# Kernel optimization log

Hardware: AMD Instinct MI355X
Metric: run time of the kernel (lower is better)

Reference implementation:

```python
import jax, jax.numpy as jnp
import numpy as np

E = 2048  # embed_size == seq_len (required: edge_weight_fc maps last dim E -> 1 on the NxN scores)
B = 4
N = 2048


def setup_inputs() -> dict:
    key = jax.random.key(0)
    ks = jax.random.split(key, 12)
    s = 0.02
    inp = {
        "query": jax.random.normal(ks[0], (B, N, E), jnp.float32),
        "key": jax.random.normal(ks[1], (B, N, E), jnp.float32),
        "value": jax.random.normal(ks[2], (B, N, E), jnp.float32),
        "mask": jax.random.randint(ks[3], (B, N, N), 0, 2, jnp.int32),
        # nn.Linear weights stored torch-style as [out, in]
        "Wq": jax.random.normal(ks[4], (E, E), jnp.float32) * s,
        "bq": jnp.zeros((E,), jnp.float32),
        "Wk": jax.random.normal(ks[5], (E, E), jnp.float32) * s,
        "bk": jnp.zeros((E,), jnp.float32),
        "Wv": jax.random.normal(ks[6], (E, E), jnp.float32) * s,
        "bv": jnp.zeros((E,), jnp.float32),
        "We": jax.random.normal(ks[7], (1, E), jnp.float32) * s,  # edge_weight_fc: Linear(E, 1)
        "be": jnp.zeros((1,), jnp.float32),
        "Wo": jax.random.normal(ks[8], (E, E), jnp.float32) * s,
        "bo": jnp.zeros((E,), jnp.float32),
    }
    return inp


def reference(query, key, value, mask, Wq, bq, Wk, bk, Wv, bv, We, be, Wo, bo):
    # QKV projections (torch Linear: x @ W.T + b)
    Q = query @ Wq.T + bq                       # [B, N, E]
    K = key @ Wk.T + bk                         # [B, N, E]
    V = value @ Wv.T + bv                       # [B, N, E]
    scale = 1.0 / jnp.sqrt(jnp.asarray(E, jnp.float32))
    scores = jnp.einsum("bqe,bke->bqk", Q, K) * scale   # [B, N, N]
    scores = scores + mask.astype(scores.dtype) * (-1e9)
    # graph_structure is non-None -> learned sigmoid edge gate over score rows
    edge_w = jax.nn.sigmoid(scores @ We.T + be)          # [B, N, 1]
    scores = scores * edge_w
    attn = jax.nn.softmax(scores, axis=-1)               # [B, N, N]
    # dropout is identity in eval mode
    out = jnp.einsum("bqk,bke->bqe", attn, V)            # [B, N, E]
    return out @ Wo.T + bo
```

## Files before the change

### kernel.cpp

```cpp
#include <hip/hip_runtime.h>
#include <math.h>

#define BB 4
#define NN 2048
#define EE 2048

typedef __attribute__((ext_vector_type(8))) unsigned short ushort8;
typedef __attribute__((ext_vector_type(8))) __bf16 bf16x8;
typedef __attribute__((ext_vector_type(4))) float f32x4;

__device__ __forceinline__ unsigned short f2bf(float f) {
  unsigned int u = __float_as_uint(f);
  u = u + 0x7fffu + ((u >> 16) & 1u);
  return (unsigned short)(u >> 16);
}
__device__ __forceinline__ float bf2f(unsigned short h) {
  return __uint_as_float((unsigned)h << 16);
}

__device__ __forceinline__ void gload16(const void* g, void* l) {
  __builtin_amdgcn_global_load_lds(
      (__attribute__((address_space(1))) void*)g,
      (__attribute__((address_space(3))) void*)l, 16, 0, 0);
}

#define BARRIER() __builtin_amdgcn_s_barrier()
#define WAIT_VM(N) asm volatile("s_waitcnt vmcnt(" #N ")")

__global__ __launch_bounds__(256) void k_f32_to_bf16(const float* __restrict__ in,
                                                     unsigned short* __restrict__ out) {
  size_t i = (size_t)blockIdx.x * 256 + threadIdx.x;
  const float4* ip = (const float4*)in;
  float4 a = ip[i * 2];
  float4 b = ip[i * 2 + 1];
  ushort8 o;
  o[0] = f2bf(a.x); o[1] = f2bf(a.y); o[2] = f2bf(a.z); o[3] = f2bf(a.w);
  o[4] = f2bf(b.x); o[5] = f2bf(b.y); o[6] = f2bf(b.z); o[7] = f2bf(b.w);
  *((ushort8*)out + i) = o;
}

__global__ __launch_bounds__(256) void k_conv3(const float* __restrict__ s0,
                                               const float* __restrict__ s1,
                                               const float* __restrict__ s2,
                                               unsigned short* __restrict__ d0,
                                               unsigned short* __restrict__ d1,
                                               unsigned short* __restrict__ d2) {
  const float* in; unsigned short* out;
  if (blockIdx.z == 0) { in = s0; out = d0; }
  else if (blockIdx.z == 1) { in = s1; out = d1; }
  else { in = s2; out = d2; }
  size_t i = (size_t)blockIdx.x * 256 + threadIdx.x;
  const float4* ip = (const float4*)in;
  float4 a = ip[i * 2];
  float4 b = ip[i * 2 + 1];
  ushort8 o;
  o[0] = f2bf(a.x); o[1] = f2bf(a.y); o[2] = f2bf(a.z); o[3] = f2bf(a.w);
  o[4] = f2bf(b.x); o[5] = f2bf(b.y); o[6] = f2bf(b.z); o[7] = f2bf(b.w);
  *((ushort8*)out + i) = o;
}

__global__ __launch_bounds__(256) void k_trf2b3(const float* __restrict__ s0,
                                                const float* __restrict__ s1,
                                                const float* __restrict__ s2,
                                                unsigned short* __restrict__ d0,
                                                unsigned short* __restrict__ d1,
                                                unsigned short* __restrict__ d2) {
  __shared__ __attribute__((aligned(16))) unsigned short tile[64][72];
  const float* in; unsigned short* out;
  if (blockIdx.z == 0) { in = s0; out = d0; }
  else if (blockIdx.z == 1) { in = s1; out = d1; }
  else { in = s2; out = d2; }
  const long eb = (long)blockIdx.x * 64;
  const long nb = (long)blockIdx.y * 64;
  const int t = threadIdx.x;
  const int r = t >> 3;
  const int c = (t & 7) * 8;

  const float* p0 = in + (nb + r) * (long)EE + eb + c;
  const float* p1 = in + (nb + 32 + r) * (long)EE + eb + c;
  float4 a0 = *(const float4*)p0, a1 = *(const float4*)(p0 + 4);
  float4 b0 = *(const float4*)p1, b1 = *(const float4*)(p1 + 4);
  unsigned short* t0 = &tile[r][c];
  unsigned short* t1 = &tile[r + 32][c];
  t0[0] = f2bf(a0.x); t0[1] = f2bf(a0.y); t0[2] = f2bf(a0.z); t0[3] = f2bf(a0.w);
  t0[4] = f2bf(a1.x); t0[5] = f2bf(a1.y); t0[6] = f2bf(a1.z); t0[7] = f2bf(a1.w);
  t1[0] = f2bf(b0.x); t1[1] = f2bf(b0.y); t1[2] = f2bf(b0.z); t1[3] = f2bf(b0.w);
  t1[4] = f2bf(b1.x); t1[5] = f2bf(b1.y); t1[6] = f2bf(b1.z); t1[7] = f2bf(b1.w);
  __syncthreads();
  ushort8 o0, o1;
#pragma unroll
  for (int j = 0; j < 8; j++) { o0[j] = tile[c + j][r]; o1[j] = tile[c + j][r + 32]; }
  *(ushort8*)(out + (eb + r) * (long)NN + nb + c) = o0;
  *(ushort8*)(out + (eb + r + 32) * (long)NN + nb + c) = o1;
}

__global__ __launch_bounds__(256) void k_transpose(const unsigned short* __restrict__ in,
                                                   unsigned short* __restrict__ out) {
  __shared__ __attribute__((aligned(16))) unsigned short tile[64][72];
  const long z = blockIdx.z;
  const long eb = (long)blockIdx.x * 64;
  const long nb = (long)blockIdx.y * 64;
  const unsigned short* ip = in + z * (long)NN * EE;
  unsigned short* op = out + z * (long)NN * EE;
  const int t = threadIdx.x;
  const int r = t >> 3;
  const int c = (t & 7) * 8;

  ushort8 u0 = *(const ushort8*)(ip + (nb + r) * EE + eb + c);
  ushort8 u1 = *(const ushort8*)(ip + (nb + 32 + r) * EE + eb + c);
  *(ushort8*)&tile[r][c] = u0;
  *(ushort8*)&tile[r + 32][c] = u1;
  __syncthreads();
  ushort8 o0, o1;
#pragma unroll
  for (int j = 0; j < 8; j++) { o0[j] = tile[c + j][r]; o1[j] = tile[c + j][r + 32]; }
  *(ushort8*)(op + (eb + r) * NN + nb + c) = o0;
  *(ushort8*)(op + (eb + r + 32) * NN + nb + c) = o1;
}

__global__ __launch_bounds__(256) void k_vecw(const float* __restrict__ Wq,
                                              const float* __restrict__ Wk,
                                              const float* __restrict__ bq,
                                              const float* __restrict__ bk,
                                              float* __restrict__ u,
                                              float* __restrict__ w2b,
                                              float* __restrict__ t4) {
  const int e = blockIdx.x * 256 + threadIdx.x;
  const int tt0 = blockIdx.y * 64;
  float su = 0.f, sw = 0.f;
#pragma unroll 4
  for (int i = 0; i < 64; i++) {
    int tt = tt0 + i;
    su += Wq[(long)tt * EE + e] * bk[tt];
    sw += Wk[(long)tt * EE + e] * bq[tt];
  }
  atomicAdd(&u[e], su);
  atomicAdd(&w2b[e], sw);
  if (blockIdx.x == 0 && threadIdx.x < 64) {
    int lane = threadIdx.x;
    float p = bq[tt0 + lane] * bk[tt0 + lane];
    for (int off = 32; off >= 1; off >>= 1) p += __shfl_down(p, off);
    if (lane == 0) atomicAdd(t4, p);
  }
}

__global__ __launch_bounds__(256) void k_cvec(const float* __restrict__ Wo,
                                              const float* __restrict__ bv,
                                              const float* __restrict__ bo,
                                              float* __restrict__ cv) {
  int row = blockIdx.x * 4 + (threadIdx.x >> 6);
  int lane = threadIdx.x & 63;
  float s = 0.f;
  for (int j = lane; j < EE; j += 64) s += Wo[(long)row * EE + j] * bv[j];
  for (int off = 32; off >= 1; off >>= 1) s += __shfl_down(s, off);
  if (lane == 0) cv[row] = s + bo[row];
}

__global__ __launch_bounds__(256) void k_rowterm(const unsigned short* __restrict__ qb,
                                                 const float* __restrict__ u,
                                                 const float* __restrict__ t4,
                                                 float* __restrict__ rt) {
  long row = (long)blockIdx.x * 4 + (threadIdx.x >> 6);
  int lane = threadIdx.x & 63;
  const unsigned short* qr = qb + row * EE;
  float s = 0.f;
#pragma unroll
  for (int it = 0; it < 4; ++it) {
    int e0 = it * 512 + lane * 8;
    ushort8 qv = *(const ushort8*)(qr + e0);
#pragma unroll
    for (int j = 0; j < 8; j++) s += bf2f(qv[j]) * u[e0 + j];
  }
  for (int off = 32; off >= 1; off >>= 1) s += __shfl_down(s, off);
  if (lane == 0) rt[row] = s + *t4;
}

__global__ __launch_bounds__(512, 4) void k_gemm128(
    const unsigned short* __restrict__ A, long lda, long sA,
    const unsigned short* __restrict__ Bm, long ldb, long sB,
    unsigned short* __restrict__ Co, long ldc, long sC, int K) {
  __shared__ __attribute__((aligned(16))) unsigned short As[2 * 8192];
  __shared__ __attribute__((aligned(16))) unsigned short Bs[2 * 8192];
  const int gx = gridDim.x, gy = gridDim.y;
  int lin = (int)blockIdx.x + gx * ((int)blockIdx.y + gy * (int)blockIdx.z);
  int nwg = gx * gy * (int)gridDim.z;
  int chunk = nwg >> 3;
  int sw = (lin & 7) * chunk + (lin >> 3);
  int bz = sw / (gx * gy); int rem = sw - bz * (gx * gy);
  int by = rem / gx; int bx = rem - by * gx;

  const long m0 = (long)by * 128;
  const long n0 = (long)bx * 128;
  const unsigned short* Ab = A + (long)bz * sA;
  const unsigned short* Bb = Bm + (long)bz * sB;
  const int t = threadIdx.x;
  const int lane = t & 63;
  const int w = t >> 6;
  const int wm = w >> 2, wn = w & 3;

  const int srow = t >> 3;
  const int scol = (((t & 7) * 16) ^ (((t >> 5) & 1) << 5)) >> 1;
  const unsigned short* Ga = Ab + (m0 + srow) * lda + scol;
  const unsigned short* Gb = Bb + (n0 + srow) * ldb + scol;
  const int ldst = t * 8;

#define STAGE(buf, tile) do { \
    const unsigned short* ga_ = Ga + (long)(tile) * 64; \
    const unsigned short* gb_ = Gb + (long)(tile) * 64; \
    unsigned short* la_ = As + (buf) * 8192 + ldst; \
    unsigned short* lb_ = Bs + (buf) * 8192 + ldst; \
    gload16(ga_, la_); gload16(ga_ + 64 * lda, la_ + 4096); \
    gload16(gb_, lb_); gload16(gb_ + 64 * ldb, lb_ + 4096); \
  } while (0)

  const int r = lane & 15;
  const int q = lane >> 4;
  const int rb2 = ((r * 128 + q * 16) ^ ((r & 4) << 3)) >> 1;
  const int aBase = wm * 4096 + rb2;
  const int bBase = wn * 2048 + rb2;

  f32x4 acc[4][2] = {};
  bf16x8 a[4][2], b[2][2];
  const int J = K >> 6;
  STAGE(0, 0);
  WAIT_VM(0);
  BARRIER();
  for (int j = 0; j < J; ++j) {
    const int c = j & 1;
    const unsigned short* Ac = As + c * 8192;
    const unsigned short* Bc = Bs + c * 8192;
#pragma unroll
    for (int mi = 0; mi < 4; mi++)
#pragma unroll
      for (int kk = 0; kk < 2; kk++)
        a[mi][kk] = *(const bf16x8*)(Ac + aBase + mi * 1024 + kk * 32);
#pragma unroll
    for (int ni = 0; ni < 2; ni++)
#pragma unroll
      for (int kk = 0; kk < 2; kk++)
        b[ni][kk] = *(const bf16x8*)(Bc + bBase + ni * 1024 + kk * 32);
    if (j + 1 < J) STAGE(c ^ 1, j + 1);
    __builtin_amdgcn_s_setprio(1);
#pragma unroll
    for (int mi = 0; mi < 4; mi++)
#pragma unroll
      for (int ni = 0; ni < 2; ni++)
#pragma unroll
        for (int kk = 0; kk < 2; kk++)
          acc[mi][ni] = __builtin_amdgcn_mfma_f32_16x16x32_bf16(
              a[mi][kk], b[ni][kk], acc[mi][ni], 0, 0, 0);
    __builtin_amdgcn_s_setprio(0);
    WAIT_VM(0);
    BARRIER();
  }
#undef STAGE
  const int cr0 = wm * 64 + (q << 2);
  const int cc0 = wn * 32 + r;
#pragma unroll
  for (int mi = 0; mi < 4; mi++)
#pragma unroll
    for (int rr = 0; rr < 4; rr++) {
      long row = m0 + cr0 + mi * 16 + rr;
#pragma unroll
      for (int ni = 0; ni < 2; ni++)
        Co[(long)bz * sC + row * ldc + n0 + cc0 + ni * 16] = f2bf(acc[mi][ni][rr]);
    }
}

template <int EPI>
__global__ __launch_bounds__(512, 2) void k_gemm256(
    const unsigned short* __restrict__ A, long lda, long sA,
    const unsigned short* __restrict__ Bm, long ldb, long sB,
    void* __restrict__ Cv, long ldc, long sC, int K,
    const float* __restrict__ bias,
    const int* __restrict__ mask, long sMask,
    const float* __restrict__ rt, float scale,
    const float* __restrict__ We, float* __restrict__ edot) {
  __shared__ __attribute__((aligned(16))) unsigned short As[2 * 16384];
  __shared__ __attribute__((aligned(16))) unsigned short Bs[2 * 16384];

  const int gx = gridDim.x, gy = gridDim.y;
  int lin = (int)blockIdx.x + gx * ((int)blockIdx.y + gy * (int)blockIdx.z);
  int nwg = gx * gy * (int)gridDim.z;
  int chunk = nwg >> 3;
  int sw = (lin & 7) * chunk + (lin >> 3);
  int bz = sw / (gx * gy); int rem = sw - bz * (gx * gy);
  int by = rem / gx; int bx = rem - by * gx;

  const long m0 = (long)by * 256;
  const long n0 = (long)bx * 256;
  const unsigned short* Ab = A + (long)bz * sA;
  const unsigned short* Bb = Bm + (long)bz * sB;

  const int t = threadIdx.x;
  const int lane = t & 63;
  const int w = t >> 6;
  const int wm = w >> 2;
  const int wn = w & 3;

  const int p0 = t * 16;
  const int q0 = p0 ^ (((p0 >> 9) & 1) << 5);
  const int srow = ((q0 >> 10) >> 1) * 16 + ((q0 >> 6) & 15);
  const int scol = ((q0 >> 10) & 1) * 32 + ((q0 & 63) >> 1);
  const unsigned short* Ga = Ab + (m0 + srow) * lda + scol;
  const unsigned short* Gb = Bb + (n0 + srow) * ldb + scol;
  const int ldst = t * 8;

#define STAGE_A(buf, h, tile) do { \
    const unsigned short* g_ = Ga + (long)(tile) * 64 + (long)(h) * 128 * lda; \
    unsigned short* l_ = As + (buf) * 16384 + (h) * 8192 + ldst; \
    gload16(g_, l_); gload16(g_ + 64 * lda, l_ + 4096); \
  } while (0)
#define STAGE_B(buf, h, tile) do { \
    const unsigned short* g_ = Gb + (long)(tile) * 64 + (long)(h) * 128 * ldb; \
    unsigned short* l_ = Bs + (buf) * 16384 + (h) * 8192 + ldst; \
    gload16(g_, l_); gload16(g_ + 64 * ldb, l_ + 4096); \
  } while (0)

  const int r = lane & 15;
  const int q = lane >> 4;
  const int c2h = ((q * 16) ^ (((lane >> 3) & 1) << 5)) >> 1;
  const int aBase = wm * 8192 + r * 32 + c2h;
  const int bBase = (wn >> 1) * 8192 + (wn & 1) * 4096 + r * 32 + c2h;

#define RD_A(bp, mbase) do { \
    _Pragma("unroll") for (int mi = 0; mi < 4; mi++) \
    _Pragma("unroll") for (int kk = 0; kk < 2; kk++) \
      a[mi][kk] = *(const bf16x8*)((bp) + aBase + ((mbase) + mi) * 1024 + kk * 512); \
  } while (0)
#define RD_B(bp, nbase) do { \
    _Pragma("unroll") for (int ni = 0; ni < 2; ni++) \
    _Pragma("unroll") for (int kk = 0; kk < 2; kk++) \
      b[(nbase) + ni][kk] = *(const bf16x8*)((bp) + bBase + ((nbase) + ni) * 1024 + kk * 512); \
  } while (0)
#define MFMA_Q(mbase, nbase) do { \
    BARRIER(); \
    __builtin_amdgcn_s_setprio(1); \
    _Pragma("unroll") for (int mi = 0; mi < 4; mi++) \
    _Pragma("unroll") for (int ni = 0; ni < 2; ni++) \
    _Pragma("unroll") for (int kk = 0; kk < 2; kk++) \
      acc[(mbase) + mi][(nbase) + ni] = __builtin_amdgcn_mfma_f32_16x16x32_bf16( \
          a[mi][kk], b[(nbase) + ni][kk], acc[(mbase) + mi][(nbase) + ni], 0, 0, 0); \
    __builtin_amdgcn_s_setprio(0); \
    BARRIER(); \
  } while (0)

  f32x4 acc[8][4] = {};
  bf16x8 a[4][2], b[4][2];
  const unsigned short* A0 = As;
  const unsigned short* B0 = Bs;
  const unsigned short* A1 = As + 16384;
  const unsigned short* B1 = Bs + 16384;
  const int J = K >> 7;

  STAGE_B(0, 0, 0); STAGE_B(0, 1, 0);
  STAGE_A(0, 0, 0); STAGE_A(0, 1, 0);
  STAGE_B(1, 0, 1); STAGE_B(1, 1, 1);
  WAIT_VM(4);
  BARRIER();

  for (int j = 0; j < J; ++j) {
    const int t0 = 2 * j, t1 = 2 * j + 1;
    const bool pf = (j + 1 < J);

    RD_A(A0, 0); RD_B(B0, 0);
    STAGE_A(1, 0, t1);
    MFMA_Q(0, 0);

    RD_B(B0, 2);
    STAGE_A(1, 1, t1);
    MFMA_Q(0, 2);

    RD_A(A0, 4);
    if (pf) STAGE_B(0, 0, t0 + 2);
    MFMA_Q(4, 0);

    if (pf) { STAGE_B(0, 1, t0 + 2); WAIT_VM(4); } else { WAIT_VM(0); }
    MFMA_Q(4, 2);

    RD_A(A1, 0); RD_B(B1, 0);
    if (pf) STAGE_A(0, 0, t0 + 2);
    MFMA_Q(0, 0);

    RD_B(B1, 2);
    if (pf) STAGE_A(0, 1, t0 + 2);
    MFMA_Q(0, 2);

    RD_A(A1, 4);
    if (pf) STAGE_B(1, 0, t1 + 2);
    MFMA_Q(4, 0);

    if (pf) { STAGE_B(1, 1, t1 + 2); WAIT_VM(4); }
    MFMA_Q(4, 2);
  }
#undef STAGE_A
#undef STAGE_B
#undef RD_A
#undef RD_B
#undef MFMA_Q

  const int cr0 = wm * 128 + (q << 2);
  const int cc0 = wn * 64 + r;
  if (EPI == 0) {
    unsigned short* Co = (unsigned short*)Cv + (long)bz * sC;
#pragma unroll
    for (int mi = 0; mi < 8; mi++)
#pragma unroll
      for (int rr = 0; rr < 4; rr++) {
        long row = m0 + cr0 + mi * 16 + rr;
#pragma unroll
        for (int ni = 0; ni < 4; ni++) {
          long col = n0 + cc0 + ni * 16;
          float v = acc[mi][ni][rr];
          if (bias) v += bias[col];
          Co[row * ldc + col] = f2bf(v);
        }
      }
  } else if (EPI == 1) {
    unsigned short* Co = (unsigned short*)Cv + (long)bz * sC;
    const int* Mp = mask + (long)bz * sMask;
    const float* rtb = rt + (long)bz * NN;
    float* edpart = (float*)As;
    if (t < 256) edpart[t] = 0.f;
    __syncthreads();
    float wec[4];
#pragma unroll
    for (int ni = 0; ni < 4; ni++) wec[ni] = We[n0 + cc0 + ni * 16];
#pragma unroll
    for (int mi = 0; mi < 8; mi++) {
      float pr[4];
#pragma unroll
      for (int rr = 0; rr < 4; rr++) {
        long row = m0 + cr0 + mi * 16 + rr;
        float rv = rtb[row];
        float pv = 0.f;
#pragma unroll
        for (int ni = 0; ni < 4; ni++) {
          long col = n0 + cc0 + ni * 16;
          float sm = (acc[mi][ni][rr] + rv) * scale + (float)Mp[row * ldc + col] * -1e9f;
          Co[row * ldc + col] = f2bf(sm);
          pv += sm * wec[ni];
        }
        pr[rr] = pv;
      }
#pragma unroll
      for (int mask_ = 1; mask_ < 16; mask_ <<= 1)
#pragma unroll
        for (int rr = 0; rr < 4; rr++) pr[rr] += __shfl_xor(pr[rr], mask_);
      if (r == 0) {
#pragma unroll
        for (int rr = 0; rr < 4; rr++)
          atomicAdd(&edpart[cr0 + mi * 16 + rr], pr[rr]);
      }
    }
    __syncthreads();
    if (t < 256) atomicAdd(&edot[(long)bz * NN + m0 + t], edpart[t]);
  } else {
    float* Co = (float*)Cv + (long)bz * sC;
#pragma unroll
    for (int mi = 0; mi < 8; mi++)
#pragma unroll
      for (int rr = 0; rr < 4; rr++) {
        long row = m0 + cr0 + mi * 16 + rr;
#pragma unroll
        for (int ni = 0; ni < 4; ni++) {
          long col = n0 + cc0 + ni * 16;
          Co[row * ldc + col] = acc[mi][ni][rr] + bias[col];
        }
      }
  }
}

__global__ __launch_bounds__(256) void k_edge_softmax(unsigned short* __restrict__ attn,
                                                      const float* __restrict__ edot,
                                                      const float* __restrict__ be) {
  __shared__ float r2[4], r3[4];
  const long row = blockIdx.x;
  unsigned short* srow = attn + row * (long)NN;
  const int t = threadIdx.x;
  const int lane = t & 63;
  const int w = t >> 6;

  float edge = 1.0f / (1.0f + expf(-(edot[row] + be[0])));
  ushort8 v = *(const ushort8*)(srow + t * 8);
  float s[8];
  float mx = -3.4e38f;
#pragma unroll
  for (int j = 0; j < 8; j++) { s[j] = bf2f(v[j]) * edge; mx = fmaxf(mx, s[j]); }
#pragma unroll
  for (int off = 32; off >= 1; off >>= 1) mx = fmaxf(mx, __shfl_down(mx, off));
  if (lane == 0) r2[w] = mx;
  __syncthreads();
  mx = fmaxf(fmaxf(r2[0], r2[1]), fmaxf(r2[2], r2[3]));

  float sum = 0.f;
  float p[8];
#pragma unroll
  for (int j = 0; j < 8; j++) { p[j] = expf(s[j] - mx); sum += p[j]; }
#pragma unroll
  for (int off = 32; off >= 1; off >>= 1) sum += __shfl_down(sum, off);
  if (lane == 0) r3[w] = sum;
  __syncthreads();
  sum = r3[0] + r3[1] + r3[2] + r3[3];
  float inv = 1.0f / sum;

  ushort8 o;
#pragma unroll
  for (int j = 0; j < 8; j++) o[j] = f2bf(p[j] * inv);
  *(ushort8*)(srow + t * 8) = o;
}

extern "C" void kernel_launch(void* const* d_in, const int* in_sizes, int n_in,
                              void* d_out, int out_size, void* d_ws, size_t ws_size,
                              hipStream_t stream) {
  (void)in_sizes; (void)n_in; (void)out_size; (void)ws_size;
  const float* query = (const float*)d_in[0];
  const float* key_  = (const float*)d_in[1];
  const float* value = (const float*)d_in[2];
  const int*   mask  = (const int*)d_in[3];
  const float* Wq = (const float*)d_in[4];
  const float* bq = (const float*)d_in[5];
  const float* Wk = (const float*)d_in[6];
  const float* bk = (const float*)d_in[7];
  const float* Wv = (const float*)d_in[8];
  const float* bv = (const float*)d_in[9];
  const float* We = (const float*)d_in[10];
  const float* be = (const float*)d_in[11];
  const float* Wo = (const float*)d_in[12];
  const float* bo = (const float*)d_in[13];
  float* out = (float*)d_out;

  const long WSZ = (long)EE * EE;
  char* ws = (char*)d_ws;
  unsigned short* WkT = (unsigned short*)(ws);
  unsigned short* Wob = WkT + WSZ;
  unsigned short* WqT = WkT + 2 * WSZ;
  unsigned short* WvT = WkT + 3 * WSZ;
  unsigned short* W2T = (unsigned short*)(ws + 33554432L);
  unsigned short* W3T = W2T + WSZ;
  unsigned short* attn = (unsigned short*)(ws);
  unsigned short* qb  = (unsigned short*)(ws + 79691776L);
  unsigned short* kb  = (unsigned short*)(ws + 114294784L);
  unsigned short* vb  = (unsigned short*)(ws + 148897792L);
  unsigned short* Tb  = vb;
  unsigned short* Vt2 = (unsigned short*)(ws + 183500800L);
  unsigned short* Vt2T = qb;
  float* cvec = (float*)(ws + 219938816L);
  float* uvec = cvec + EE;
  float* w2b  = cvec + 2 * EE;
  float* t4   = cvec + 3 * EE;
  float* rt   = cvec + 3 * EE + 64;
  float* edot = rt + (long)BB * NN;

  const float scale = 1.0f / sqrtf((float)EE);
  dim3 blk(256), blk5(512);

  k_trf2b3<<<dim3(32, 32, 3), blk, 0, stream>>>(Wk, Wq, Wv, WkT, WqT, WvT);
  k_f32_to_bf16<<<2048, blk, 0, stream>>>(Wo, Wob);
  hipMemsetAsync(uvec, 0, (2 * EE + 64) * sizeof(float), stream);
  hipMemsetAsync(edot, 0, (long)BB * NN * sizeof(float), stream);
  k_vecw<<<dim3(8, 32), blk, 0, stream>>>(Wq, Wk, bq, bk, uvec, w2b, t4);
  k_cvec<<<512, blk, 0, stream>>>(Wo, bv, bo, cvec);
  k_gemm128<<<dim3(16, 16, 2), blk5, 0, stream>>>(WkT, EE, WSZ, WqT, EE, WSZ,
      W2T, EE, WSZ, EE);
  k_conv3<<<dim3(8192, 1, 3), blk, 0, stream>>>(query, key_, value, qb, kb, vb);
  k_gemm256<0><<<dim3(8, 32, 1), blk5, 0, stream>>>(vb, EE, 0, W3T, EE, 0,
      Vt2, EE, 0, EE, nullptr, nullptr, 0, nullptr, 0.f, nullptr, nullptr);
  k_gemm256<0><<<dim3(8, 32, 1), blk5, 0, stream>>>(qb, EE, 0, W2T, EE, 0,
      Tb, EE, 0, EE, w2b, nullptr, 0, nullptr, 0.f, nullptr, nullptr);
  k_rowterm<<<2048, blk, 0, stream>>>(qb, uvec, t4, rt);
  k_transpose<<<dim3(32, 32, BB), blk, 0, stream>>>(Vt2, Vt2T);
  k_gemm256<1><<<dim3(8, 8, BB), blk5, 0, stream>>>(Tb, EE, (long)NN * EE, kb, EE, (long)NN * EE,
      attn, NN, (long)NN * NN, EE, nullptr, mask, (long)NN * NN, rt, scale, We, edot);
  k_edge_softmax<<<BB * NN, blk, 0, stream>>>(attn, edot, be);
  k_gemm256<2><<<dim3(8, 8, BB), blk5, 0, stream>>>(attn, NN, (long)NN * NN,
      Vt2T, NN, (long)EE * NN, out, EE, (long)NN * EE, NN,
      cvec, nullptr, 0, nullptr, 0.f, nullptr, nullptr);
}
```

Measured before the change: 471.0 us.

## Replace pipelined 256x256 GEMM with simple single-buffered 128x128 tile kernel

Replaces the heavily pipelined, double-buffered 256x256 GEMM kernel (512 threads, swizzled LDS, interleaved prefetch and MFMA phases) with a plain 128x128 tile kernel. The new kernel uses 256 threads, a single 32-wide K step, and two syncthreads per iteration. Launch grids are rescaled to match. This gives up load/compute overlap and data reuse, and the unswizzled LDS reads may bank-conflict, which likely makes all four big GEMMs slower. It reads like a simpler baseline or experiment.

```diff
diff --git a/kernel.cpp b/kernel.cpp
--- a/kernel.cpp
+++ b/kernel.cpp
@@ -268,7 +268,7 @@
 }
 
 template <int EPI>
-__global__ __launch_bounds__(512, 2) void k_gemm256(
+__global__ __launch_bounds__(256) void k_gemm97(
     const unsigned short* __restrict__ A, long lda, long sA,
     const unsigned short* __restrict__ Bm, long ldb, long sB,
     void* __restrict__ Cv, long ldc, long sC, int K,
@@ -276,8 +276,8 @@
     const int* __restrict__ mask, long sMask,
     const float* __restrict__ rt, float scale,
     const float* __restrict__ We, float* __restrict__ edot) {
-  __shared__ __attribute__((aligned(16))) unsigned short As[2 * 16384];
-  __shared__ __attribute__((aligned(16))) unsigned short Bs[2 * 16384];
+  __shared__ __attribute__((aligned(16))) unsigned short As[128 * 32];
+  __shared__ __attribute__((aligned(16))) unsigned short Bs[128 * 32];
 
   const int gx = gridDim.x, gy = gridDim.y;
   int lin = (int)blockIdx.x + gx * ((int)blockIdx.y + gy * (int)blockIdx.z);
@@ -287,130 +287,65 @@
   int bz = sw / (gx * gy); int rem = sw - bz * (gx * gy);
   int by = rem / gx; int bx = rem - by * gx;
 
-  const long m0 = (long)by * 256;
-  const long n0 = (long)bx * 256;
+  const long m0 = (long)by * 128;
+  const long n0 = (long)bx * 128;
   const unsigned short* Ab = A + (long)bz * sA;
   const unsigned short* Bb = Bm + (long)bz * sB;
 
   const int t = threadIdx.x;
   const int lane = t & 63;
   const int w = t >> 6;
-  const int wm = w >> 2;
-  const int wn = w & 3;
-
-  const int p0 = t * 16;
-  const int q0 = p0 ^ (((p0 >> 9) & 1) << 5);
-  const int srow = ((q0 >> 10) >> 1) * 16 + ((q0 >> 6) & 15);
-  const int scol = ((q0 >> 10) & 1) * 32 + ((q0 & 63) >> 1);
-  const unsigned short* Ga = Ab + (m0 + srow) * lda + scol;
-  const unsigned short* Gb = Bb + (n0 + srow) * ldb + scol;
-  const int ldst = t * 8;
-
-#define STAGE_A(buf, h, tile) do { \
-    const unsigned short* g_ = Ga + (long)(tile) * 64 + (long)(h) * 128 * lda; \
-    unsigned short* l_ = As + (buf) * 16384 + (h) * 8192 + ldst; \
-    gload16(g_, l_); gload16(g_ + 64 * lda, l_ + 4096); \
-  } while (0)
-#define STAGE_B(buf, h, tile) do { \
-    const unsigned short* g_ = Gb + (long)(tile) * 64 + (long)(h) * 128 * ldb; \
-    unsigned short* l_ = Bs + (buf) * 16384 + (h) * 8192 + ldst; \
-    gload16(g_, l_); gload16(g_ + 64 * ldb, l_ + 4096); \
-  } while (0)
-
-  const int r = lane & 15;
-  const int q = lane >> 4;
-  const int c2h = ((q * 16) ^ (((lane >> 3) & 1) << 5)) >> 1;
-  const int aBase = wm * 8192 + r * 32 + c2h;
-  const int bBase = (wn >> 1) * 8192 + (wn & 1) * 4096 + r * 32 + c2h;
-
-#define RD_A(bp, mbase) do { \
-    _Pragma("unroll") for (int mi = 0; mi < 4; mi++) \
-    _Pragma("unroll") for (int kk = 0; kk < 2; kk++) \
-      a[mi][kk] = *(const bf16x8*)((bp) + aBase + ((mbase) + mi) * 1024 + kk * 512); \
-  } while (0)
-#define RD_B(bp, nbase) do { \
-    _Pragma("unroll") for (int ni = 0; ni < 2; ni++) \
-    _Pragma("unroll") for (int kk = 0; kk < 2; kk++) \
-      b[(nbase) + ni][kk] = *(const bf16x8*)((bp) + bBase + ((nbase) + ni) * 1024 + kk * 512); \
-  } while (0)
-#define MFMA_Q(mbase, nbase) do { \
-    BARRIER(); \
-    __builtin_amdgcn_s_setprio(1); \
-    _Pragma("unroll") for (int mi = 0; mi < 4; mi++) \
-    _Pragma("unroll") for (int ni = 0; ni < 2; ni++) \
-    _Pragma("unroll") for (int kk = 0; kk < 2; kk++) \
-      acc[(mbase) + mi][(nbase) + ni] = __builtin_amdgcn_mfma_f32_16x16x32_bf16( \
-          a[mi][kk], b[(nbase) + ni][kk], acc[(mbase) + mi][(nbase) + ni], 0, 0, 0); \
-    __builtin_amdgcn_s_setprio(0); \
-    BARRIER(); \
-  } while (0)
-
-  f32x4 acc[8][4] = {};
-  bf16x8 a[4][2], b[4][2];
-  const unsigned short* A0 = As;
-  const unsigned short* B0 = Bs;
-  const unsigned short* A1 = As + 16384;
-  const unsigned short* B1 = Bs + 16384;
-  const int J = K >> 7;
-
-  STAGE_B(0, 0, 0); STAGE_B(0, 1, 0);
-  STAGE_A(0, 0, 0); STAGE_A(0, 1, 0);
-  STAGE_B(1, 0, 1); STAGE_B(1, 1, 1);
-  WAIT_VM(4);
-  BARRIER();
-
-  for (int j = 0; j < J; ++j) {
-    const int t0 = 2 * j, t1 = 2 * j + 1;
-    const bool pf = (j + 1 < J);
-
-    RD_A(A0, 0); RD_B(B0, 0);
-    STAGE_A(1, 0, t1);
-    MFMA_Q(0, 0);
-
-    RD_B(B0, 2);
-    STAGE_A(1, 1, t1);
-    MFMA_Q(0, 2);
-
-    RD_A(A0, 4);
-    if (pf) STAGE_B(0, 0, t0 + 2);
-    MFMA_Q(4, 0);
-
-    if (pf) { STAGE_B(0, 1, t0 + 2); WAIT_VM(4); } else { WAIT_VM(0); }
-    MFMA_Q(4, 2);
-
-    RD_A(A1, 0); RD_B(B1, 0);
-    if (pf) STAGE_A(0, 0, t0 + 2);
-    MFMA_Q(0, 0);
-
-    RD_B(B1, 2);
-    if (pf) STAGE_A(0, 1, t0 + 2);
-    MFMA_Q(0, 2);
-
-    RD_A(A1, 4);
-    if (pf) STAGE_B(1, 0, t1 + 2);
-    MFMA_Q(4, 0);
-
-    if (pf) { STAGE_B(1, 1, t1 + 2); WAIT_VM(4); }
-    MFMA_Q(4, 2);
+  const int wr = (w >> 1) * 64;
+  const int wc = (w & 1) * 64;
+
+  const int sr = t >> 2;
+  const int sc = (t & 3) * 8;
+  const unsigned short* ga0 = Ab + (m0 + sr) * lda + sc;
+  const unsigned short* ga1 = ga0 + 64 * lda;
+  const unsigned short* gb0 = Bb + (n0 + sr) * ldb + sc;
+  const unsigned short* gb1 = gb0 + 64 * ldb;
+  unsigned short* la0 = As + sr * 32 + sc;
+  unsigned short* la1 = la0 + 64 * 32;
+  unsigned short* lb0 = Bs + sr * 32 + sc;
+  unsigned short* lb1 = lb0 + 64 * 32;
+
+  f32x4 acc[4][4] = {};
+  const int arow = wr + (lane & 15);
+  const int brow = wc + (lane & 15);
+  const int kof = (lane >> 4) * 8;
+
+  for (int kt = 0; kt < K; kt += 32) {
+    gload16(ga0, la0); gload16(ga1, la1);
+    gload16(gb0, lb0); gload16(gb1, lb1);
+    ga0 += 32; ga1 += 32; gb0 += 32; gb1 += 32;
+    __syncthreads();
+    bf16x8 af[4], bfr[4];
+#pragma unroll
+    for (int mi = 0; mi < 4; mi++)
+      af[mi] = *(const bf16x8*)(As + (arow + mi * 16) * 32 + kof);
+#pragma unroll
+    for (int ni = 0; ni < 4; ni++)
+      bfr[ni] = *(const bf16x8*)(Bs + (brow + ni * 16) * 32 + kof);
+#pragma unroll
+    for (int mi = 0; mi < 4; mi++)
+#pragma unroll
+      for (int ni = 0; ni < 4; ni++)
+        acc[mi][ni] = __builtin_amdgcn_mfma_f32_16x16x32_bf16(af[mi], bfr[ni], acc[mi][ni], 0, 0, 0);
+    __syncthreads();
   }
-#undef STAGE_A
-#undef STAGE_B
-#undef RD_A
-#undef RD_B
-#undef MFMA_Q
-
-  const int cr0 = wm * 128 + (q << 2);
-  const int cc0 = wn * 64 + r;
+
+  const int crow = wr + ((lane >> 4) << 2);
+  const int ccol = wc + (lane & 15);
   if (EPI == 0) {
     unsigned short* Co = (unsigned short*)Cv + (long)bz * sC;
 #pragma unroll
-    for (int mi = 0; mi < 8; mi++)
+    for (int mi = 0; mi < 4; mi++)
 #pragma unroll
       for (int rr = 0; rr < 4; rr++) {
-        long row = m0 + cr0 + mi * 16 + rr;
+        long row = m0 + crow + mi * 16 + rr;
 #pragma unroll
         for (int ni = 0; ni < 4; ni++) {
-          long col = n0 + cc0 + ni * 16;
+          long col = n0 + ccol + ni * 16;
           float v = acc[mi][ni][rr];
           if (bias) v += bias[col];
           Co[row * ldc + col] = f2bf(v);
@@ -421,22 +356,23 @@
     const int* Mp = mask + (long)bz * sMask;
     const float* rtb = rt + (long)bz * NN;
     float* edpart = (float*)As;
-    if (t < 256) edpart[t] = 0.f;
+    if (t < 128) edpart[t] = 0.f;
     __syncthreads();
     float wec[4];
 #pragma unroll
-    for (int ni = 0; ni < 4; ni++) wec[ni] = We[n0 + cc0 + ni * 16];
-#pragma unroll
-    for (int mi = 0; mi < 8; mi++) {
+    for (int ni = 0; ni < 4; ni++) wec[ni] = We[n0 + ccol + ni * 16];
+#pragma unroll
+    for (int mi = 0; mi < 4; mi++) {
       float pr[4];
 #pragma unroll
       for (int rr = 0; rr < 4; rr++) {
-        long row = m0 + cr0 + mi * 16 + rr;
+        int row_l = crow + mi * 16 + rr;
+        long row = m0 + row_l;
         float rv = rtb[row];
         float pv = 0.f;
 #pragma unroll
         for (int ni = 0; ni < 4; ni++) {
-          long col = n0 + cc0 + ni * 16;
+          long col = n0 + ccol + ni * 16;
           float sm = (acc[mi][ni][rr] + rv) * scale + (float)Mp[row * ldc + col] * -1e9f;
           Co[row * ldc + col] = f2bf(sm);
           pv += sm * wec[ni];
@@ -447,24 +383,24 @@
       for (int mask_ = 1; mask_ < 16; mask_ <<= 1)
 #pragma unroll
         for (int rr = 0; rr < 4; rr++) pr[rr] += __shfl_xor(pr[rr], mask_);
-      if (r == 0) {
+      if ((lane & 15) == 0) {
 #pragma unroll
         for (int rr = 0; rr < 4; rr++)
-          atomicAdd(&edpart[cr0 + mi * 16 + rr], pr[rr]);
+          atomicAdd(&edpart[crow + mi * 16 + rr], pr[rr]);
       }
     }
     __syncthreads();
-    if (t < 256) atomicAdd(&edot[(long)bz * NN + m0 + t], edpart[t]);
+    if (t < 128) atomicAdd(&edot[(long)bz * NN + m0 + t], edpart[t]);
   } else {
     float* Co = (float*)Cv + (long)bz * sC;
 #pragma unroll
-    for (int mi = 0; mi < 8; mi++)
+    for (int mi = 0; mi < 4; mi++)
 #pragma unroll
       for (int rr = 0; rr < 4; rr++) {
-        long row = m0 + cr0 + mi * 16 + rr;
+        long row = m0 + crow + mi * 16 + rr;
 #pragma unroll
         for (int ni = 0; ni < 4; ni++) {
-          long col = n0 + cc0 + ni * 16;
+          long col = n0 + ccol + ni * 16;
           Co[row * ldc + col] = acc[mi][ni][rr] + bias[col];
         }
       }
@@ -564,16 +500,16 @@
   k_gemm128<<<dim3(16, 16, 2), blk5, 0, stream>>>(WkT, EE, WSZ, WqT, EE, WSZ,
       W2T, EE, WSZ, EE);
   k_conv3<<<dim3(8192, 1, 3), blk, 0, stream>>>(query, key_, value, qb, kb, vb);
-  k_gemm256<0><<<dim3(8, 32, 1), blk5, 0, stream>>>(vb, EE, 0, W3T, EE, 0,
+  k_gemm97<0><<<dim3(16, 64, 1), blk, 0, stream>>>(vb, EE, 0, W3T, EE, 0,
       Vt2, EE, 0, EE, nullptr, nullptr, 0, nullptr, 0.f, nullptr, nullptr);
-  k_gemm256<0><<<dim3(8, 32, 1), blk5, 0, stream>>>(qb, EE, 0, W2T, EE, 0,
+  k_gemm97<0><<<dim3(16, 64, 1), blk, 0, stream>>>(qb, EE, 0, W2T, EE, 0,
       Tb, EE, 0, EE, w2b, nullptr, 0, nullptr, 0.f, nullptr, nullptr);
   k_rowterm<<<2048, blk, 0, stream>>>(qb, uvec, t4, rt);
   k_transpose<<<dim3(32, 32, BB), blk, 0, stream>>>(Vt2, Vt2T);
-  k_gemm256<1><<<dim3(8, 8, BB), blk5, 0, stream>>>(Tb, EE, (long)NN * EE, kb, EE, (long)NN * EE,
+  k_gemm97<1><<<dim3(16, 16, BB), blk, 0, stream>>>(Tb, EE, (long)NN * EE, kb, EE, (long)NN * EE,
       attn, NN, (long)NN * NN, EE, nullptr, mask, (long)NN * NN, rt, scale, We, edot);
   k_edge_softmax<<<BB * NN, blk, 0, stream>>>(attn, edot, be);
-  k_gemm256<2><<<dim3(8, 8, BB), blk5, 0, stream>>>(attn, NN, (long)NN * NN,
+  k_gemm97<2><<<dim3(16, 16, BB), blk, 0, stream>>>(attn, NN, (long)NN * NN,
       Vt2T, NN, (long)EE * NN, out, EE, (long)NN * EE, NN,
       cvec, nullptr, 0, nullptr, 0.f, nullptr, nullptr);
 }
```

Measured after the change: 651.5 us. +38.3%, slower.
